# Kernel tuning notes

Hardware: AMD Instinct MI355X
Metric: run time of the kernel (lower is better)

## Reference

```python
import jax, jax.numpy as jnp
import numpy as np

H = W = 224


def setup_inputs() -> dict:
    key = jax.random.key(0)
    k1, k2, k3, k4 = jax.random.split(key, 4)
    B = 64
    depth = jax.random.uniform(k1, (B, 1, H, W), dtype=jnp.float32)
    object_channel = jax.random.uniform(k2, (B, 1, H, W), dtype=jnp.float32)
    gaze = jax.random.normal(k3, (B, 3), dtype=jnp.float32)
    head_point = jax.random.randint(k4, (B, 2), 0, 224, dtype=jnp.int64)
    return {"depth": depth, "object_channel": object_channel, "gaze": gaze, "head_point": head_point}


def reference(depth, object_channel, gaze, head_point):
    B = depth.shape[0]
    d = depth * object_channel                      # [B,1,H,W]
    # per-batch depth band width: (max - min) / 24
    fd_range = (jnp.max(d, axis=(1, 2, 3)) - jnp.min(d, axis=(1, 2, 3))) / 24.0  # [B]
    # depth at head point (hp0 indexes rows, hp1 indexes cols, as in torch code)
    hp0 = head_point[:, 0].astype(jnp.int32)
    hp1 = head_point[:, 1].astype(jnp.int32)
    head_depth = d[jnp.arange(B), 0, hp0, hp1]      # [B]
    point_depth = head_depth + gaze[:, 2] * 224.0   # [B]

    pd = point_depth[:, None, None, None]
    fr = fd_range[:, None, None, None]

    def band(m):
        # where(pd - m*fr <= d <= pd + m*fr, d, 0)
        return jnp.where((pd - m * fr <= d) & (pd + m * fr >= d), d, 0.0)

    fd_0, fd_1, fd_2 = band(1.0), band(2.0), band(3.0)

    # gaze cone mask: angle between (pixel - head_point) and gaze xy
    xy = gaze[:, :2]                                # [B,2]
    hp0f = head_point[:, 0].astype(jnp.float32)[:, None, None]
    hp1f = head_point[:, 1].astype(jnp.float32)[:, None, None]
    # arr = [k, i] - head_point  (k = col index, i = row index)
    arr0 = jnp.arange(W, dtype=jnp.float32)[None, None, :] - hp0f   # [B,H,W]
    arr1 = jnp.arange(H, dtype=jnp.float32)[None, :, None] - hp1f   # [B,H,W]
    dot = arr0 * xy[:, 0, None, None] + arr1 * xy[:, 1, None, None]
    denom = jnp.sqrt(arr0 ** 2 + arr1 ** 2) * jnp.sqrt(xy[:, 0] ** 2 + xy[:, 1] ** 2)[:, None, None]
    ang = jnp.arccos(dot / denom)                   # nan at head pixel / out-of-range cos
    mask = jnp.nan_to_num(jnp.maximum(1.0 - 12.0 * ang / jnp.pi, 0.0))[:, None, :, :]  # [B,1,H,W]

    x_0 = fd_0 * mask
    x_1 = fd_1 * mask
    x_2 = fd_2 * mask
    return jnp.concatenate([x_0, x_1, x_2], axis=1)  # [B,3,H,W]
```

## Files before the change

### kernel.cpp

```cpp
#include <hip/hip_runtime.h>
#include <math.h>

#define HW   224
#define NPIX (HW * HW)
#define NB   64
#define NBPB 8

typedef float fx4 __attribute__((ext_vector_type(4)));

__global__ __launch_bounds__(256) void reduce_minmax(const float* __restrict__ depth,
                                                     const float* __restrict__ obj,
                                                     float* __restrict__ ws) {
    const int b    = blockIdx.x / NBPB;
    const int part = blockIdx.x % NBPB;
    const int floats_per_part = NPIX / NBPB;
    const int vec_per_part    = floats_per_part / 4;

    const fx4* d4 = (const fx4*)(depth + (size_t)b * NPIX + part * floats_per_part);
    const fx4* o4 = (const fx4*)(obj   + (size_t)b * NPIX + part * floats_per_part);

    float vmin = INFINITY, vmax = -INFINITY;
    for (int idx = threadIdx.x; idx < vec_per_part; idx += 256) {
        fx4 dd = d4[idx];
        fx4 oo = o4[idx];
        float p0 = dd.x * oo.x, p1 = dd.y * oo.y, p2 = dd.z * oo.z, p3 = dd.w * oo.w;
        vmin = fminf(vmin, fminf(fminf(p0, p1), fminf(p2, p3)));
        vmax = fmaxf(vmax, fmaxf(fmaxf(p0, p1), fmaxf(p2, p3)));
    }

    #pragma unroll
    for (int off = 32; off > 0; off >>= 1) {
        vmin = fminf(vmin, __shfl_down(vmin, off, 64));
        vmax = fmaxf(vmax, __shfl_down(vmax, off, 64));
    }
    __shared__ float smin[4], smax[4];
    const int wave = threadIdx.x >> 6;
    const int lane = threadIdx.x & 63;
    if (lane == 0) { smin[wave] = vmin; smax[wave] = vmax; }
    __syncthreads();
    if (threadIdx.x == 0) {
        float m0 = fminf(fminf(smin[0], smin[1]), fminf(smin[2], smin[3]));
        float m1 = fmaxf(fmaxf(smax[0], smax[1]), fmaxf(smax[2], smax[3]));
        ws[b * NBPB + part]             = m0;
        ws[NB * NBPB + b * NBPB + part] = m1;
    }
}

__global__ __launch_bounds__(256) void fused_band_mask(const float* __restrict__ depth,
                                                       const float* __restrict__ obj,
                                                       const float* __restrict__ gaze,
                                                       const int* __restrict__ head_point,
                                                       const float* __restrict__ ws,
                                                       float* __restrict__ out) {
#pragma clang fp contract(off)
    const int b = blockIdx.y;
    const int t = blockIdx.x * 256 + threadIdx.x;
    const int p = t * 4;
    const int i = p / HW;
    const int j = p % HW;

    float mn = INFINITY, mx = -INFINITY;
    #pragma unroll
    for (int k = 0; k < NBPB; ++k) {
        mn = fminf(mn, ws[b * NBPB + k]);
        mx = fmaxf(mx, ws[NB * NBPB + b * NBPB + k]);
    }
    const float fr = (mx - mn) / 24.0f;

    const int hp0 = head_point[2 * b];
    const int hp1 = head_point[2 * b + 1];
    const float gx = gaze[3 * b], gy = gaze[3 * b + 1], gz = gaze[3 * b + 2];

    const size_t ibase = (size_t)b * NPIX;
    const float head_d = depth[ibase + hp0 * HW + hp1] * obj[ibase + hp0 * HW + hp1];
    const float pd  = head_d + gz * 224.0f;
    const float nxy = sqrtf(gx * gx + gy * gy);
    const float PI32 = 3.14159274101257324f;

    const float t1 = 1.0f * fr, t2 = 2.0f * fr, t3 = 3.0f * fr;
    const float lo1 = pd - t1, hi1 = pd + t1;
    const float lo2 = pd - t2, hi2 = pd + t2;
    const float lo3 = pd - t3, hi3 = pd + t3;

    fx4 dd = *(const fx4*)(depth + ibase + p);
    fx4 oo = *(const fx4*)(obj   + ibase + p);
    float dv[4] = { dd.x * oo.x, dd.y * oo.y, dd.z * oo.z, dd.w * oo.w };

    const float hp0f = (float)hp0, hp1f = (float)hp1;
    const float arr1 = (float)i - hp1f;

    float x0[4], x1[4], x2[4];
    #pragma unroll
    for (int k = 0; k < 4; ++k) {
        const float arr0  = (float)(j + k) - hp0f;
        const float dot   = arr0 * gx + arr1 * gy;
        const float denom = sqrtf(arr0 * arr0 + arr1 * arr1) * nxy;
        const float ang   = acosf(dot / denom);
        float mk = fmaxf(1.0f - (12.0f * ang) / PI32, 0.0f);
        if (isnan(mk)) mk = 0.0f;
        const float d  = dv[k];
        const float dm = d * mk;
        x0[k] = (lo1 <= d && hi1 >= d) ? dm : 0.0f;
        x1[k] = (lo2 <= d && hi2 >= d) ? dm : 0.0f;
        x2[k] = (lo3 <= d && hi3 >= d) ? dm : 0.0f;
    }

    const size_t obase = (size_t)b * 3 * NPIX + p;
    fx4 v0 = { x0[0], x0[1], x0[2], x0[3] };
    fx4 v1 = { x1[0], x1[1], x1[2], x1[3] };
    fx4 v2 = { x2[0], x2[1], x2[2], x2[3] };
    __builtin_nontemporal_store(v0, (fx4*)(out + obase));
    __builtin_nontemporal_store(v1, (fx4*)(out + obase + NPIX));
    __builtin_nontemporal_store(v2, (fx4*)(out + obase + 2 * NPIX));
}

extern "C" void kernel_launch(void* const* d_in, const int* in_sizes, int n_in,
                              void* d_out, int out_size, void* d_ws, size_t ws_size,
                              hipStream_t stream) {
    const float* depth      = (const float*)d_in[0];
    const float* obj        = (const float*)d_in[1];
    const float* gaze       = (const float*)d_in[2];
    const int*   head_point = (const int*)d_in[3];
    float* out = (float*)d_out;
    float* ws  = (float*)d_ws;

    reduce_minmax<<<NB * NBPB, 256, 0, stream>>>(depth, obj, ws);
    fused_band_mask<<<dim3(49, NB), 256, 0, stream>>>(depth, obj, gaze, head_point, ws, out);
}
```

Before: 93.24 us.

## Skip input loads and acos for wavefronts entirely outside the gaze cone

```diff
diff --git a/kernel.cpp b/kernel.cpp
--- a/kernel.cpp
+++ b/kernel.cpp
@@ -4,15 +4,15 @@
 #define HW   224
 #define NPIX (HW * HW)
 #define NB   64
-#define NBPB 8
+#define NBPB 16
 
 typedef float fx4 __attribute__((ext_vector_type(4)));
 
 __global__ __launch_bounds__(256) void reduce_minmax(const float* __restrict__ depth,
                                                      const float* __restrict__ obj,
                                                      float* __restrict__ ws) {
-    const int b    = blockIdx.x / NBPB;
-    const int part = blockIdx.x % NBPB;
+    const int b    = blockIdx.x >> 4;
+    const int part = blockIdx.x & 15;
     const int floats_per_part = NPIX / NBPB;
     const int vec_per_part    = floats_per_part / 4;
 
@@ -41,8 +41,8 @@
     if (threadIdx.x == 0) {
         float m0 = fminf(fminf(smin[0], smin[1]), fminf(smin[2], smin[3]));
         float m1 = fmaxf(fmaxf(smax[0], smax[1]), fmaxf(smax[2], smax[3]));
-        ws[b * NBPB + part]             = m0;
-        ws[NB * NBPB + b * NBPB + part] = m1;
+        ws[b * NBPB + part]              = m0;
+        ws[NB * NBPB + b * NBPB + part]  = m1;
     }
 }
 
@@ -55,9 +55,42 @@
 #pragma clang fp contract(off)
     const int b = blockIdx.y;
     const int t = blockIdx.x * 256 + threadIdx.x;
-    const int p = t * 4;
+    if (t >= NPIX / 8) return;
+    const int p = t * 8;
     const int i = p / HW;
     const int j = p % HW;
+
+    const int hp0 = head_point[2 * b];
+    const int hp1 = head_point[2 * b + 1];
+    const float gx = gaze[3 * b], gy = gaze[3 * b + 1];
+
+    const float hp0f = (float)hp0, hp1f = (float)hp1;
+    const float arr1 = (float)i - hp1f;
+    const float nxy  = sqrtf(gx * gx + gy * gy);
+    const float PI32 = 3.14159274101257324f;
+
+    float r[8];
+    bool anyl = false;
+    #pragma unroll
+    for (int k = 0; k < 8; ++k) {
+        const float arr0  = (float)(j + k) - hp0f;
+        const float dot   = arr0 * gx + arr1 * gy;
+        const float denom = sqrtf(arr0 * arr0 + arr1 * arr1) * nxy;
+        r[k] = dot / denom;
+        anyl = anyl || (r[k] > 0.96f);
+    }
+
+    const size_t obase = (size_t)b * 3 * NPIX + p;
+    if (!__any(anyl)) {
+        const fx4 z = { 0.0f, 0.0f, 0.0f, 0.0f };
+        __builtin_nontemporal_store(z, (fx4*)(out + obase));
+        __builtin_nontemporal_store(z, (fx4*)(out + obase + 4));
+        __builtin_nontemporal_store(z, (fx4*)(out + obase + NPIX));
+        __builtin_nontemporal_store(z, (fx4*)(out + obase + NPIX + 4));
+        __builtin_nontemporal_store(z, (fx4*)(out + obase + 2 * NPIX));
+        __builtin_nontemporal_store(z, (fx4*)(out + obase + 2 * NPIX + 4));
+        return;
+    }
 
     float mn = INFINITY, mx = -INFINITY;
     #pragma unroll
@@ -67,35 +100,27 @@
     }
     const float fr = (mx - mn) / 24.0f;
 
-    const int hp0 = head_point[2 * b];
-    const int hp1 = head_point[2 * b + 1];
-    const float gx = gaze[3 * b], gy = gaze[3 * b + 1], gz = gaze[3 * b + 2];
-
+    const float gz = gaze[3 * b + 2];
     const size_t ibase = (size_t)b * NPIX;
     const float head_d = depth[ibase + hp0 * HW + hp1] * obj[ibase + hp0 * HW + hp1];
-    const float pd  = head_d + gz * 224.0f;
-    const float nxy = sqrtf(gx * gx + gy * gy);
-    const float PI32 = 3.14159274101257324f;
+    const float pd = head_d + gz * 224.0f;
 
     const float t1 = 1.0f * fr, t2 = 2.0f * fr, t3 = 3.0f * fr;
     const float lo1 = pd - t1, hi1 = pd + t1;
     const float lo2 = pd - t2, hi2 = pd + t2;
     const float lo3 = pd - t3, hi3 = pd + t3;
 
-    fx4 dd = *(const fx4*)(depth + ibase + p);
-    fx4 oo = *(const fx4*)(obj   + ibase + p);
-    float dv[4] = { dd.x * oo.x, dd.y * oo.y, dd.z * oo.z, dd.w * oo.w };
+    fx4 dd0 = *(const fx4*)(depth + ibase + p);
+    fx4 dd1 = *(const fx4*)(depth + ibase + p + 4);
+    fx4 oo0 = *(const fx4*)(obj   + ibase + p);
+    fx4 oo1 = *(const fx4*)(obj   + ibase + p + 4);
+    float dv[8] = { dd0.x * oo0.x, dd0.y * oo0.y, dd0.z * oo0.z, dd0.w * oo0.w,
+                    dd1.x * oo1.x, dd1.y * oo1.y, dd1.z * oo1.z, dd1.w * oo1.w };
 
-    const float hp0f = (float)hp0, hp1f = (float)hp1;
-    const float arr1 = (float)i - hp1f;
-
-    float x0[4], x1[4], x2[4];
+    float x0[8], x1[8], x2[8];
     #pragma unroll
-    for (int k = 0; k < 4; ++k) {
-        const float arr0  = (float)(j + k) - hp0f;
-        const float dot   = arr0 * gx + arr1 * gy;
-        const float denom = sqrtf(arr0 * arr0 + arr1 * arr1) * nxy;
-        const float ang   = acosf(dot / denom);
+    for (int k = 0; k < 8; ++k) {
+        const float ang = acosf(r[k]);
         float mk = fmaxf(1.0f - (12.0f * ang) / PI32, 0.0f);
         if (isnan(mk)) mk = 0.0f;
         const float d  = dv[k];
@@ -105,13 +130,13 @@
         x2[k] = (lo3 <= d && hi3 >= d) ? dm : 0.0f;
     }
 
-    const size_t obase = (size_t)b * 3 * NPIX + p;
-    fx4 v0 = { x0[0], x0[1], x0[2], x0[3] };
-    fx4 v1 = { x1[0], x1[1], x1[2], x1[3] };
-    fx4 v2 = { x2[0], x2[1], x2[2], x2[3] };
-    __builtin_nontemporal_store(v0, (fx4*)(out + obase));
-    __builtin_nontemporal_store(v1, (fx4*)(out + obase + NPIX));
-    __builtin_nontemporal_store(v2, (fx4*)(out + obase + 2 * NPIX));
+    fx4 v;
+    v = (fx4){ x0[0], x0[1], x0[2], x0[3] }; __builtin_nontemporal_store(v, (fx4*)(out + obase));
+    v = (fx4){ x0[4], x0[5], x0[6], x0[7] }; __builtin_nontemporal_store(v, (fx4*)(out + obase + 4));
+    v = (fx4){ x1[0], x1[1], x1[2], x1[3] }; __builtin_nontemporal_store(v, (fx4*)(out + obase + NPIX));
+    v = (fx4){ x1[4], x1[5], x1[6], x1[7] }; __builtin_nontemporal_store(v, (fx4*)(out + obase + NPIX + 4));
+    v = (fx4){ x2[0], x2[1], x2[2], x2[3] }; __builtin_nontemporal_store(v, (fx4*)(out + obase + 2 * NPIX));
+    v = (fx4){ x2[4], x2[5], x2[6], x2[7] }; __builtin_nontemporal_store(v, (fx4*)(out + obase + 2 * NPIX + 4));
 }
 
 extern "C" void kernel_launch(void* const* d_in, const int* in_sizes, int n_in,
@@ -125,5 +150,5 @@
     float* ws  = (float*)d_ws;
 
     reduce_minmax<<<NB * NBPB, 256, 0, stream>>>(depth, obj, ws);
-    fused_band_mask<<<dim3(49, NB), 256, 0, stream>>>(depth, obj, gaze, head_point, ws, out);
+    fused_band_mask<<<dim3((NPIX / 8 + 255) / 256, NB), 256, 0, stream>>>(depth, obj, gaze, head_point, ws, out);
 }
```

Measured after the change: 93.13 us. Within noise of the previous version (-0.1%).
